# Kernel optimization log

Measured on AMD Instinct MI355X. Metric: run time of the kernel, lower is better.

## Reference

```python
import jax, jax.numpy as jnp
import numpy as np

STU_N, EXER_N, K_N, EMB = 20000, 20000, 128, 128
BATCH = 4096

def _pos(w):
    # PosLinear weight transform: 2*relu(-w) + w  (== |w|)
    return 2.0 * jax.nn.relu(-w) + w

def setup_inputs() -> dict:
    key = jax.random.key(0)
    ks = jax.random.split(key, 12)
    xav = lambda k, shape: jax.random.normal(k, shape, jnp.float32) * np.sqrt(2.0 / sum(shape))
    return {
        "stu_id": jax.random.randint(ks[0], (BATCH,), 0, STU_N, jnp.int32),
        "exer_id": jax.random.randint(ks[1], (BATCH,), 0, EXER_N, jnp.int32),
        "kq": jax.random.uniform(ks[2], (BATCH, K_N), jnp.float32),
        "student_q": xav(ks[3], (STU_N, EMB)),
        "exercise_k": xav(ks[4], (EXER_N, EMB)),
        "student_v": xav(ks[5], (STU_N, EMB)),
        "exercise_v": xav(ks[6], (EXER_N, EMB)),
        "knowledge_v": xav(ks[7], (K_N, EMB)),
        "W1": xav(ks[8], (EMB, 2 * EMB)), "b1": jnp.zeros((EMB,), jnp.float32),
        "W2": xav(ks[9], (EMB, 2 * EMB)), "b2": jnp.zeros((EMB,), jnp.float32),
        "W3": xav(ks[10], (1, EMB)), "b3": jnp.zeros((1,), jnp.float32),
    }

def reference(stu_id, exer_id, kq, student_q, exercise_k, student_v, exercise_v,
              knowledge_v, W1, b1, W2, b2, W3, b3):
    stu_q = student_q[stu_id]          # (B, D)
    exer_k = exercise_k[exer_id]       # (B, D)
    stu_v = student_v[stu_id]          # (B, D)
    exer_v = exercise_v[exer_id]       # (B, D)
    B, D = stu_v.shape
    K = knowledge_v.shape[0]

    kn = jnp.broadcast_to(knowledge_v[None, :, :], (B, K, D))
    stu_b = jnp.broadcast_to(stu_v[:, None, :], (B, K, D))
    exer_b = jnp.broadcast_to(exer_v[:, None, :], (B, K, D))

    # PosLinear 1/2 on concat([x, kn]) -> split GEMM avoids materializing concat
    W1p, W2p, W3p = _pos(W1), _pos(W2), _pos(W3)
    pref = jax.nn.sigmoid(jnp.einsum('bkd,ed->bke', jnp.concatenate([stu_b, kn], -1), W1p) + b1)
    diff = jax.nn.sigmoid(jnp.einsum('bkd,ed->bke', jnp.concatenate([exer_b, kn], -1), W2p) + b2)

    disc = jax.nn.sigmoid(stu_q * exer_k)              # (B, D)
    input_x = (pref - diff) * disc[:, None, :]         # (B, K, D)
    o = jax.nn.sigmoid(jnp.einsum('bkd,od->bko', input_x, W3p) + b3)  # (B, K, 1)

    sum_out = jnp.sum(o * kq[:, :, None], axis=1)      # (B, 1)
    count = jnp.sum(kq, axis=1, keepdims=True)         # (B, 1)
    return jnp.squeeze(sum_out / count)                # (B,)
```

## Files before the change

kernel.cpp:

```cpp
#include <hip/hip_runtime.h>

#define D  128
#define KN 128
#define NB 16
#define LOG2E 1.44269504088896340736f

typedef float f32x4  __attribute__((ext_vector_type(4)));
typedef float f32x16 __attribute__((ext_vector_type(16)));
typedef short s16x8  __attribute__((ext_vector_type(8)));

__device__ __forceinline__ float negexp(float v) {
    return __builtin_amdgcn_exp2f(v * -LOG2E);
}
__device__ __forceinline__ float sigf(float x) {
    return __builtin_amdgcn_rcpf(1.0f + negexp(x));
}
__device__ __forceinline__ unsigned short f2bf(float f) {
    unsigned u = __float_as_uint(f);
    return (unsigned short)((u + 0x7fffu + ((u >> 16) & 1u)) >> 16);
}
__device__ __forceinline__ s16x8 pack8(float4 a, float4 b) {
    s16x8 r;
    r[0]=(short)f2bf(a.x); r[1]=(short)f2bf(a.y); r[2]=(short)f2bf(a.z); r[3]=(short)f2bf(a.w);
    r[4]=(short)f2bf(b.x); r[5]=(short)f2bf(b.y); r[6]=(short)f2bf(b.z); r[7]=(short)f2bf(b.w);
    return r;
}
__device__ __forceinline__ s16x8 pack8abs(float4 a, float4 b) {
    s16x8 r;
    r[0]=(short)f2bf(fabsf(a.x)); r[1]=(short)f2bf(fabsf(a.y)); r[2]=(short)f2bf(fabsf(a.z)); r[3]=(short)f2bf(fabsf(a.w));
    r[4]=(short)f2bf(fabsf(b.x)); r[5]=(short)f2bf(fabsf(b.y)); r[6]=(short)f2bf(fabsf(b.z)); r[7]=(short)f2bf(fabsf(b.w));
    return r;
}

#define CORE(EA1, EA2, T, PZ, A0, A1) do {                                   \
    float x0_ = fmaf((EA1), (T).x, 1.0f);                                    \
    float x1_ = fmaf((EA1), (T).y, 1.0f);                                    \
    float y0_ = fmaf((EA2), (T).z, 1.0f);                                    \
    float y1_ = fmaf((EA2), (T).w, 1.0f);                                    \
    (A0) = fmaf((y0_ - x0_) * (PZ), __builtin_amdgcn_rcpf(x0_ * y0_), (A0)); \
    (A1) = fmaf((y1_ - x1_) * (PZ), __builtin_amdgcn_rcpf(x1_ * y1_), (A1)); \
} while (0)

#define TWRITE(T, ACC) {                                                      \
    const int idx_ = (wid << 2) + (T);                                        \
    const int et_ = (idx_ >> 2) & 3, kt_ = idx_ & 3;                          \
    const int slot_ = (idx_ < 16) ? 0 : 2;                                    \
    const float* bias_ = (idx_ < 16) ? b1 : b2;                               \
    const int k_ = kt_ * 32 + l31;                                            \
    const int kof_ = ((k_ >> 1) << 2) + (k_ & 1) + slot_;                     \
    _Pragma("unroll")                                                         \
    for (int r = 0; r < 16; ++r) {                                            \
        int e_ = et_ * 32 + (r & 3) + ((r >> 2) << 3) + (g32 << 2);           \
        TABf[e_ * 256 + kof_] = negexp(ACC[r] + bias_[e_]);                   \
    } }

__global__ __launch_bounds__(512, 1) void fused_kernel(
    const int* __restrict__ stu_id, const int* __restrict__ exer_id,
    const float* __restrict__ kq,
    const float* __restrict__ stu_q, const float* __restrict__ exer_k,
    const float* __restrict__ stu_v, const float* __restrict__ exer_v,
    const float* __restrict__ kn,
    const float* __restrict__ W1, const float* __restrict__ b1,
    const float* __restrict__ W2, const float* __restrict__ b2,
    const float* __restrict__ W3, const float* __restrict__ b3,
    float* __restrict__ out, int B)
{
    __shared__ float4 smem4[9728];
    __shared__ int sids[NB], eids[NB];

    float* TABf = (float*)smem4;
    float* EAf  = TABf + 32768;
    float* PZf  = EAf + 4096;
    char* KNs_base = (char*)smem4;
    char* W1s_base = KNs_base + 32768;
    char* W2s_base = KNs_base + 65536;

    const int tid  = threadIdx.x;
    const int b0   = blockIdx.x * NB;
    const int lane = tid & 63, wid = tid >> 6;
    const int l31 = lane & 31, g32 = lane >> 5;
    const int l15 = lane & 15, g16 = lane >> 4;

    if (tid < NB) {
        int b = b0 + tid;
        sids[tid] = stu_id[b < B ? b : 0];
        eids[tid] = exer_id[b < B ? b : 0];
    }
    for (int i = tid; i < 128 * 16; i += 512) {
        int row = i >> 4, c = i & 15;
        int byt = row * 256 + (((c << 4)) ^ ((row & 7) << 4));
        const float4* sk = (const float4*)(kn + (size_t)row * D + c * 8);
        *(s16x8*)(KNs_base + byt) = pack8(sk[0], sk[1]);
        const float4* s1 = (const float4*)(W1 + (size_t)row * (2 * D) + D + c * 8);
        *(s16x8*)(W1s_base + byt) = pack8abs(s1[0], s1[1]);
        const float4* s2 = (const float4*)(W2 + (size_t)row * (2 * D) + D + c * 8);
        *(s16x8*)(W2s_base + byt) = pack8abs(s2[0], s2[1]);
    }
    __syncthreads();

    const int sid_l = sids[l15], eid_l = eids[l15];
    const int erow  = wid * 16 + l15;
    float4 ga[8], ge[8];
    #pragma unroll
    for (int q = 0; q < 4; ++q) {
        int d = q * 32 + g16 * 8;
        const float4* pa = (const float4*)(stu_v + (size_t)sid_l * D + d);
        ga[2*q] = pa[0]; ga[2*q+1] = pa[1];
        const float4* pe = (const float4*)(exer_v + (size_t)eid_l * D + d);
        ge[2*q] = pe[0]; ge[2*q+1] = pe[1];
    }

    f32x16 t0acc = {0}, t1acc = {0}, t2acc = {0}, t3acc = {0};
    {
        const char* Wsb = (wid < 4) ? W1s_base : W2s_base;
        const int er = (wid & 3) * 32 + l31;
        const int eswz = (er & 7) << 4;
        const int kswz = (l31 & 7) << 4;
        #pragma unroll
        for (int q = 0; q < 8; ++q) {
            int dby = q * 32 + g32 * 16;
            s16x8 a_  = *(const s16x8*)(Wsb + er * 256 + (dby ^ eswz));
            s16x8 bb0 = *(const s16x8*)(KNs_base + (  0 + l31) * 256 + (dby ^ kswz));
            s16x8 bb1 = *(const s16x8*)(KNs_base + ( 32 + l31) * 256 + (dby ^ kswz));
            s16x8 bb2 = *(const s16x8*)(KNs_base + ( 64 + l31) * 256 + (dby ^ kswz));
            s16x8 bb3 = *(const s16x8*)(KNs_base + ( 96 + l31) * 256 + (dby ^ kswz));
            t0acc = __builtin_amdgcn_mfma_f32_32x32x16_bf16(a_, bb0, t0acc, 0, 0, 0);
            t1acc = __builtin_amdgcn_mfma_f32_32x32x16_bf16(a_, bb1, t1acc, 0, 0, 0);
            t2acc = __builtin_amdgcn_mfma_f32_32x32x16_bf16(a_, bb2, t2acc, 0, 0, 0);
            t3acc = __builtin_amdgcn_mfma_f32_32x32x16_bf16(a_, bb3, t3acc, 0, 0, 0);
        }
    }

    f32x4 accS = {0, 0, 0, 0}, accE = {0, 0, 0, 0};
    #pragma unroll
    for (int q = 0; q < 4; ++q) {
        int d = q * 32 + g16 * 8;
        const float4* pb = (const float4*)(W1 + (size_t)erow * (2 * D) + d);
        accS = __builtin_amdgcn_mfma_f32_16x16x32_bf16(
            pack8(ga[2*q], ga[2*q+1]), pack8abs(pb[0], pb[1]), accS, 0, 0, 0);
        const float4* pc = (const float4*)(W2 + (size_t)erow * (2 * D) + d);
        accE = __builtin_amdgcn_mfma_f32_16x16x32_bf16(
            pack8(ge[2*q], ge[2*q+1]), pack8abs(pc[0], pc[1]), accE, 0, 0, 0);
    }
    #pragma unroll
    for (int r = 0; r < 4; ++r) {
        int b = g16 * 4 + r;
        int eo = b * 256 + 2 * erow;
        EAf[eo]     = negexp(accS[r]);
        EAf[eo + 1] = negexp(accE[r]);
    }
    {
        int b = tid >> 5, e4 = (tid & 31) << 2;
        float4 sq = *(const float4*)(stu_q + (size_t)sids[b] * D + e4);
        float4 ek = *(const float4*)(exer_k + (size_t)eids[b] * D + e4);
        float4 w3 = *(const float4*)(W3 + e4);
        float4 z;
        z.x = sigf(sq.x * ek.x) * fabsf(w3.x);
        z.y = sigf(sq.y * ek.y) * fabsf(w3.y);
        z.z = sigf(sq.z * ek.z) * fabsf(w3.z);
        z.w = sigf(sq.w * ek.w) * fabsf(w3.w);
        *(float4*)(PZf + b * D + e4) = z;
    }
    __syncthreads();

    TWRITE(0, t0acc) TWRITE(1, t1acc) TWRITE(2, t2acc) TWRITE(3, t3acc)
    __syncthreads();

    const float4* TAB4 = (const float4*)TABf;
    const float4* EA4  = (const float4*)EAf;
    const float2* PZ2  = (const float2*)PZf;

    float2 acc[16];
    #pragma unroll
    for (int r = 0; r < 16; ++r) acc[r] = make_float2(0.f, 0.f);

    for (int jj = 0; jj < 8; ++jj) {
        const int e0 = wid * 16 + 2 * jj;
        const int jg = wid * 8 + jj;
        float4 t0 = TAB4[e0 * 64 + lane];
        float4 t1 = TAB4[(e0 + 1) * 64 + lane];
        #pragma unroll
        for (int r = 0; r < 16; ++r) {
            float4 eA = EA4[r * 64 + jg];
            float2 zA = PZ2[r * 64 + jg];
            CORE(eA.x, eA.y, t0, zA.x, acc[r].x, acc[r].y);
            CORE(eA.z, eA.w, t1, zA.y, acc[r].x, acc[r].y);
        }
    }
    __syncthreads();

    float2* RED = (float2*)TABf;
    #pragma unroll
    for (int r = 0; r < 16; ++r)
        RED[(wid * 16 + r) * 64 + lane] = acc[r];
    __syncthreads();

    const float b3v = b3[0];
    const int rA = 2 * wid, rB = 2 * wid + 1;
    const int bA = b0 + rA, bB = b0 + rB;

    float2 sA = make_float2(0.f, 0.f), sB = make_float2(0.f, 0.f);
    #pragma unroll
    for (int w = 0; w < 8; ++w) {
        float2 pA = RED[(w * 16 + rA) * 64 + lane];
        float2 pB = RED[(w * 16 + rB) * 64 + lane];
        sA.x += pA.x; sA.y += pA.y;
        sB.x += pB.x; sB.y += pB.y;
    }

    float o0a = sigf(sA.x + b3v), o1a = sigf(sA.y + b3v);
    float o0b = sigf(sB.x + b3v), o1b = sigf(sB.y + b3v);
    float na = 0.f, da = 0.f, nb = 0.f, db = 0.f;
    if (bA < B) {
        float2 kqa = *(const float2*)(kq + (size_t)bA * D + 2 * lane);
        na = fmaf(o0a, kqa.x, o1a * kqa.y); da = kqa.x + kqa.y;
    }
    if (bB < B) {
        float2 kqb = *(const float2*)(kq + (size_t)bB * D + 2 * lane);
        nb = fmaf(o0b, kqb.x, o1b * kqb.y); db = kqb.x + kqb.y;
    }
    #pragma unroll
    for (int off = 32; off > 0; off >>= 1) {
        na += __shfl_xor(na, off); da += __shfl_xor(da, off);
        nb += __shfl_xor(nb, off); db += __shfl_xor(db, off);
    }
    if (lane == 0) {
        if (bA < B) out[bA] = na / da;
        if (bB < B) out[bB] = nb / db;
    }
}

extern "C" void kernel_launch(void* const* d_in, const int* in_sizes, int n_in,
                              void* d_out, int out_size, void* d_ws, size_t ws_size,
                              hipStream_t stream)
{
    const int*   stu_id      = (const int*)  d_in[0];
    const int*   exer_id     = (const int*)  d_in[1];
    const float* kq          = (const float*)d_in[2];
    const float* student_q   = (const float*)d_in[3];
    const float* exercise_k  = (const float*)d_in[4];
    const float* student_v   = (const float*)d_in[5];
    const float* exercise_v  = (const float*)d_in[6];
    const float* knowledge_v = (const float*)d_in[7];
    const float* W1 = (const float*)d_in[8];
    const float* b1 = (const float*)d_in[9];
    const float* W2 = (const float*)d_in[10];
    const float* b2 = (const float*)d_in[11];
    const float* W3 = (const float*)d_in[12];
    const float* b3 = (const float*)d_in[13];
    float* out = (float*)d_out;
    const int B = in_sizes[0];

    int nblk = (B + NB - 1) / NB;
    fused_kernel<<<nblk, 512, 0, stream>>>(
        stu_id, exer_id, kq, student_q, exercise_k, student_v, exercise_v,
        knowledge_v, W1, b1, W2, b2, W3, b3, out, B);
}
```

Before: 31.43 us.

## Load GEMM operands straight from global and broadcast per-row scalars via readlane

Drops the LDS staging of bf16 knowledge and weight tiles, along with the first barrier. Each wave now reads fp32 operands directly from global memory and converts them to bf16 in registers before the MFMAs. The per-(batch, e) exp terms and the disc*|W3| values stay in registers and are broadcast with readlane in the inner loop, replacing the LDS EA/PZ tables and one more barrier. This cuts shared-memory footprint and synchronisation, at the cost of redundant global loads and conversions per wave and many scalar readlane ops in the hot loop.

```diff
diff --git a/kernel.cpp b/kernel.cpp
--- a/kernel.cpp
+++ b/kernel.cpp
@@ -30,6 +30,9 @@
     r[0]=(short)f2bf(fabsf(a.x)); r[1]=(short)f2bf(fabsf(a.y)); r[2]=(short)f2bf(fabsf(a.z)); r[3]=(short)f2bf(fabsf(a.w));
     r[4]=(short)f2bf(fabsf(b.x)); r[5]=(short)f2bf(fabsf(b.y)); r[6]=(short)f2bf(fabsf(b.z)); r[7]=(short)f2bf(fabsf(b.w));
     return r;
+}
+__device__ __forceinline__ float rl(float v, int srcLane) {
+    return __uint_as_float(__builtin_amdgcn_readlane(__float_as_uint(v), srcLane));
 }
 
 #define CORE(EA1, EA2, T, PZ, A0, A1) do {                                   \
@@ -65,41 +68,19 @@
     const float* __restrict__ W3, const float* __restrict__ b3,
     float* __restrict__ out, int B)
 {
-    __shared__ float4 smem4[9728];
-    __shared__ int sids[NB], eids[NB];
-
+    __shared__ float4 smem4[8192];
     float* TABf = (float*)smem4;
-    float* EAf  = TABf + 32768;
-    float* PZf  = EAf + 4096;
-    char* KNs_base = (char*)smem4;
-    char* W1s_base = KNs_base + 32768;
-    char* W2s_base = KNs_base + 65536;
 
     const int tid  = threadIdx.x;
     const int b0   = blockIdx.x * NB;
     const int lane = tid & 63, wid = tid >> 6;
     const int l31 = lane & 31, g32 = lane >> 5;
     const int l15 = lane & 15, g16 = lane >> 4;
-
-    if (tid < NB) {
-        int b = b0 + tid;
-        sids[tid] = stu_id[b < B ? b : 0];
-        eids[tid] = exer_id[b < B ? b : 0];
-    }
-    for (int i = tid; i < 128 * 16; i += 512) {
-        int row = i >> 4, c = i & 15;
-        int byt = row * 256 + (((c << 4)) ^ ((row & 7) << 4));
-        const float4* sk = (const float4*)(kn + (size_t)row * D + c * 8);
-        *(s16x8*)(KNs_base + byt) = pack8(sk[0], sk[1]);
-        const float4* s1 = (const float4*)(W1 + (size_t)row * (2 * D) + D + c * 8);
-        *(s16x8*)(W1s_base + byt) = pack8abs(s1[0], s1[1]);
-        const float4* s2 = (const float4*)(W2 + (size_t)row * (2 * D) + D + c * 8);
-        *(s16x8*)(W2s_base + byt) = pack8abs(s2[0], s2[1]);
-    }
-    __syncthreads();
-
-    const int sid_l = sids[l15], eid_l = eids[l15];
-    const int erow  = wid * 16 + l15;
+    const int bmax = B - 1;
+
+    const int bl = b0 + l15;
+    const int sid_l = stu_id[bl <= bmax ? bl : bmax];
+    const int eid_l = exer_id[bl <= bmax ? bl : bmax];
     float4 ga[8], ge[8];
     #pragma unroll
     for (int q = 0; q < 4; ++q) {
@@ -112,25 +93,29 @@
 
     f32x16 t0acc = {0}, t1acc = {0}, t2acc = {0}, t3acc = {0};
     {
-        const char* Wsb = (wid < 4) ? W1s_base : W2s_base;
+        const float* Wt = (wid < 4) ? W1 : W2;
         const int er = (wid & 3) * 32 + l31;
-        const int eswz = (er & 7) << 4;
-        const int kswz = (l31 & 7) << 4;
         #pragma unroll
         for (int q = 0; q < 8; ++q) {
-            int dby = q * 32 + g32 * 16;
-            s16x8 a_  = *(const s16x8*)(Wsb + er * 256 + (dby ^ eswz));
-            s16x8 bb0 = *(const s16x8*)(KNs_base + (  0 + l31) * 256 + (dby ^ kswz));
-            s16x8 bb1 = *(const s16x8*)(KNs_base + ( 32 + l31) * 256 + (dby ^ kswz));
-            s16x8 bb2 = *(const s16x8*)(KNs_base + ( 64 + l31) * 256 + (dby ^ kswz));
-            s16x8 bb3 = *(const s16x8*)(KNs_base + ( 96 + l31) * 256 + (dby ^ kswz));
-            t0acc = __builtin_amdgcn_mfma_f32_32x32x16_bf16(a_, bb0, t0acc, 0, 0, 0);
-            t1acc = __builtin_amdgcn_mfma_f32_32x32x16_bf16(a_, bb1, t1acc, 0, 0, 0);
-            t2acc = __builtin_amdgcn_mfma_f32_32x32x16_bf16(a_, bb2, t2acc, 0, 0, 0);
-            t3acc = __builtin_amdgcn_mfma_f32_32x32x16_bf16(a_, bb3, t3acc, 0, 0, 0);
+            int del = q * 16 + g32 * 8;
+            const float4* pw = (const float4*)(Wt + (size_t)er * (2 * D) + D + del);
+            s16x8 a_ = pack8abs(pw[0], pw[1]);
+            const float4* pk0 = (const float4*)(kn + (size_t)(  0 + l31) * D + del);
+            const float4* pk1 = (const float4*)(kn + (size_t)( 32 + l31) * D + del);
+            const float4* pk2 = (const float4*)(kn + (size_t)( 64 + l31) * D + del);
+            const float4* pk3 = (const float4*)(kn + (size_t)( 96 + l31) * D + del);
+            s16x8 f0 = pack8(pk0[0], pk0[1]);
+            s16x8 f1 = pack8(pk1[0], pk1[1]);
+            s16x8 f2 = pack8(pk2[0], pk2[1]);
+            s16x8 f3 = pack8(pk3[0], pk3[1]);
+            t0acc = __builtin_amdgcn_mfma_f32_32x32x16_bf16(a_, f0, t0acc, 0, 0, 0);
+            t1acc = __builtin_amdgcn_mfma_f32_32x32x16_bf16(a_, f1, t1acc, 0, 0, 0);
+            t2acc = __builtin_amdgcn_mfma_f32_32x32x16_bf16(a_, f2, t2acc, 0, 0, 0);
+            t3acc = __builtin_amdgcn_mfma_f32_32x32x16_bf16(a_, f3, t3acc, 0, 0, 0);
         }
     }
 
+    const int erow = wid * 16 + l15;
     f32x4 accS = {0, 0, 0, 0}, accE = {0, 0, 0, 0};
     #pragma unroll
     for (int q = 0; q < 4; ++q) {
@@ -142,49 +127,41 @@
         accE = __builtin_amdgcn_mfma_f32_16x16x32_bf16(
             pack8(ge[2*q], ge[2*q+1]), pack8abs(pc[0], pc[1]), accE, 0, 0, 0);
     }
-    #pragma unroll
-    for (int r = 0; r < 4; ++r) {
-        int b = g16 * 4 + r;
-        int eo = b * 256 + 2 * erow;
-        EAf[eo]     = negexp(accS[r]);
-        EAf[eo + 1] = negexp(accE[r]);
-    }
+    float eS[4], eE[4], pzr[4];
+    #pragma unroll
+    for (int r = 0; r < 4; ++r) { eS[r] = negexp(accS[r]); eE[r] = negexp(accE[r]); }
     {
-        int b = tid >> 5, e4 = (tid & 31) << 2;
-        float4 sq = *(const float4*)(stu_q + (size_t)sids[b] * D + e4);
-        float4 ek = *(const float4*)(exer_k + (size_t)eids[b] * D + e4);
-        float4 w3 = *(const float4*)(W3 + e4);
-        float4 z;
-        z.x = sigf(sq.x * ek.x) * fabsf(w3.x);
-        z.y = sigf(sq.y * ek.y) * fabsf(w3.y);
-        z.z = sigf(sq.z * ek.z) * fabsf(w3.z);
-        z.w = sigf(sq.w * ek.w) * fabsf(w3.w);
-        *(float4*)(PZf + b * D + e4) = z;
-    }
-    __syncthreads();
+        const int e = wid * 16 + l15;
+        const float w3a = fabsf(W3[e]);
+        #pragma unroll
+        for (int r = 0; r < 4; ++r) {
+            int b = b0 + g16 * 4 + r; b = b <= bmax ? b : bmax;
+            float sq = stu_q[(size_t)stu_id[b] * D + e];
+            float ek = exer_k[(size_t)exer_id[b] * D + e];
+            pzr[r] = sigf(sq * ek) * w3a;
+        }
+    }
 
     TWRITE(0, t0acc) TWRITE(1, t1acc) TWRITE(2, t2acc) TWRITE(3, t3acc)
     __syncthreads();
 
     const float4* TAB4 = (const float4*)TABf;
-    const float4* EA4  = (const float4*)EAf;
-    const float2* PZ2  = (const float2*)PZf;
-
     float2 acc[16];
     #pragma unroll
     for (int r = 0; r < 16; ++r) acc[r] = make_float2(0.f, 0.f);
 
     for (int jj = 0; jj < 8; ++jj) {
-        const int e0 = wid * 16 + 2 * jj;
-        const int jg = wid * 8 + jj;
-        float4 t0 = TAB4[e0 * 64 + lane];
-        float4 t1 = TAB4[(e0 + 1) * 64 + lane];
+        const int el0 = 2 * jj, el1 = 2 * jj + 1;
+        float4 t0 = TAB4[(wid * 16 + el0) * 64 + lane];
+        float4 t1 = TAB4[(wid * 16 + el1) * 64 + lane];
         #pragma unroll
         for (int r = 0; r < 16; ++r) {
-            float4 eA = EA4[r * 64 + jg];
-            float2 zA = PZ2[r * 64 + jg];
-            CORE(eA.x, eA.y, t0, zA.x, acc[r].x, acc[r].y);
-            CORE(eA.z, eA.w, t1, zA.y, acc[r].x, acc[r].y);
+            const int s0 = el0 + 16 * (r >> 2);
+            const int s1 = el1 + 16 * (r >> 2);
+            float a10 = rl(eS[r & 3], s0), a20 = rl(eE[r & 3], s0), z0 = rl(pzr[r & 3], s0);
+            float a11 = rl(eS[r & 3], s1), a21 = rl(eE[r & 3], s1), z1 = rl(pzr[r & 3], s1);
+            CORE(a10, a20, t0, z0, acc[r].x, acc[r].y);
+            CORE(a11, a21, t1, z1, acc[r].x, acc[r].y);
         }
     }
     __syncthreads();
```

Result: slower. 53.26 us (+69.5%).
